# Optimization experiments

Hardware: AMD Instinct MI355X
Metric: run time of the kernel (lower is better)

## Reference

```python
import jax, jax.numpy as jnp
import numpy as np

B, S, E = 32, 577, 1024
H = 16
D = E // H  # head_size = 64


def setup_inputs() -> dict:
    key = jax.random.key(0)
    ks = jax.random.split(key, 5)
    scale_init = E ** -0.5
    x = jax.random.normal(ks[0], (B, S, E), dtype=jnp.float32)
    # Per-head projection weights. torch Linear weight is [out,in]; we store
    # [H, E, D] so that x @ Wq[h] == torch_linear(x) with weight Wq[h].T.
    Wq = jax.random.normal(ks[1], (H, E, D), dtype=jnp.float32) * scale_init
    Wk = jax.random.normal(ks[2], (H, E, D), dtype=jnp.float32) * scale_init
    Wv = jax.random.normal(ks[3], (H, E, D), dtype=jnp.float32) * scale_init
    # Output projection (with bias, as in nn.Linear default)
    Wo = jax.random.normal(ks[4], (E, E), dtype=jnp.float32) * scale_init
    bo = jnp.zeros((E,), dtype=jnp.float32)
    return {"x": x, "Wq": Wq, "Wk": Wk, "Wv": Wv, "Wo": Wo, "bo": bo}


def reference(x, Wq, Wk, Wv, Wo, bo):
    scale = D ** -0.5
    # Per-head QKV projections, vectorized over heads: [B,H,S,D]
    q = jnp.einsum('bse,hed->bhsd', x, Wq)
    k = jnp.einsum('bse,hed->bhsd', x, Wk)
    v = jnp.einsum('bse,hed->bhsd', x, Wv)
    scores = jnp.einsum('bhsd,bhtd->bhst', q, k) * scale  # [B,H,S,S]
    attn = jax.nn.softmax(scores, axis=-1)
    out = jnp.einsum('bhst,bhtd->bhsd', attn, v)  # [B,H,S,D]
    # Concat heads: head h occupies slice [h*D:(h+1)*D], matching torch.cat order
    out = out.transpose(0, 2, 1, 3).reshape(B, S, E)
    return out @ Wo.T + bo  # torch Linear: x @ W.T + b
```

## Files before the change

### kernel.cpp

```cpp
#include <hip/hip_runtime.h>
#include <hip/hip_bf16.h>
#include <stdint.h>

using sh8    = __attribute__((ext_vector_type(8))) short;
using f32x4  = __attribute__((ext_vector_type(4))) float;
using f32x16 = __attribute__((ext_vector_type(16))) float;

#define MFMA16(a, b, c) __builtin_amdgcn_mfma_f32_16x16x32_bf16(a, b, c, 0, 0, 0)
#define EXP2F(x) __builtin_amdgcn_exp2f(x)
#define PRIO1() __builtin_amdgcn_s_setprio(1)
#define PRIO0() __builtin_amdgcn_s_setprio(0)

static constexpr int BB = 32, SS = 577, HH = 16;
static constexpr int MM = BB * SS;
static constexpr int SPAD = 640;
static constexpr float QSCALE = 0.18033688011112042f;

__device__ __forceinline__ ushort f2b(float f) {
  union { float f; uint32_t u; } v{f};
  uint32_t r = v.u + 0x7FFFu + ((v.u >> 16) & 1u);
  return (ushort)(r >> 16);
}

__device__ __forceinline__ float bf2f(ushort u) {
  union { uint32_t u; float f; } v{(uint32_t)u << 16};
  return v.f;
}

#if __has_builtin(__builtin_amdgcn_cvt_pk_bf16_f32)
typedef __attribute__((ext_vector_type(2))) __bf16 bf16x2_t;
__device__ __forceinline__ uint32_t pk_bf16(float a, float b) {
  union { bf16x2_t v; uint32_t u; } c;
  c.v = __builtin_amdgcn_cvt_pk_bf16_f32(a, b);
  return c.u;
}
#else
__device__ __forceinline__ uint32_t pk_bf16(float a, float b) {
  return (uint32_t)f2b(a) | ((uint32_t)f2b(b) << 16);
}
#endif

__device__ __forceinline__ void gld16(const ushort* g, ushort* l) {
  __builtin_amdgcn_global_load_lds(
      (const __attribute__((address_space(1))) uint32_t*)g,
      (__attribute__((address_space(3))) uint32_t*)l, 16, 0, 0);
}

__global__ __launch_bounds__(256)
void convert2_f32_bf16(const float* __restrict__ a, ushort* __restrict__ oa, int na4,
                       const float* __restrict__ b, ushort* __restrict__ ob, int nb4) {
  const int total = na4 + nb4;
  const int stride = gridDim.x * 256;
  for (int i = blockIdx.x * 256 + threadIdx.x; i < total; i += stride) {
    const float4 f = (i < na4) ? ((const float4*)a)[i] : ((const float4*)b)[i - na4];
    ushort4 u;
    u.x = f2b(f.x); u.y = f2b(f.y); u.z = f2b(f.z); u.w = f2b(f.w);
    if (i < na4) ((ushort4*)oa)[i] = u;
    else         ((ushort4*)ob)[i - na4] = u;
  }
}

__global__ __launch_bounds__(256)
void convert_wqkv(const float* __restrict__ Wq, const float* __restrict__ Wk,
                  const float* __restrict__ Wv, ushort* __restrict__ Wt) {
  __shared__ ushort T[64 * 72];
  const int tid = threadIdx.x;
  const int kt = blockIdx.x, sh = blockIdx.y;
  const int sel = sh >> 4, h = sh & 15;
  const float* W = (sel == 0) ? Wq : ((sel == 1) ? Wk : Wv);
  const float qs = (sel == 0) ? QSCALE : 1.0f;
  const int rr = tid >> 4;
  const int rc = (tid & 15) * 4;
#pragma unroll
  for (int p = 0; p < 64; p += 16) {
    const float4 f = *(const float4*)(W + (size_t)h * 65536 + (size_t)(kt * 64 + p + rr) * 64 + rc);
    ushort4 u;
    u.x = f2b(f.x * qs); u.y = f2b(f.y * qs); u.z = f2b(f.z * qs); u.w = f2b(f.w * qs);
    *(ushort4*)&T[(p + rr) * 72 + rc] = u;
  }
  __syncthreads();
  const int dd = tid >> 2;
  const int c16 = (tid & 3) * 16;
  sh8 v0, v1;
#pragma unroll
  for (int j = 0; j < 8; j++) v0[j] = (short)T[(c16 + j) * 72 + dd];
#pragma unroll
  for (int j = 0; j < 8; j++) v1[j] = (short)T[(c16 + 8 + j) * 72 + dd];
  ushort* op = Wt + ((size_t)sel * 1024 + h * 64 + dd) * 1024 + kt * 64 + c16;
  *(sh8*)op = v0;
  *(sh8*)(op + 8) = v1;
}

template <int MODE>
__global__ __launch_bounds__(256)
void gemm_bt(const ushort* __restrict__ A, const ushort* __restrict__ Bt,
             ushort* __restrict__ Cb, float* __restrict__ Cf,
             const float* __restrict__ bias, int M, int N, int K) {
  __shared__ ushort Al[128 * 64];
  __shared__ ushort Bl[128 * 64];
  const int tid = threadIdx.x;
  const int lane = tid & 63, w = tid >> 6;
  const int l15 = lane & 15, quad = lane >> 4;
  const int wm = (w >> 1) * 64, wn = (w & 1) * 64;
  const int m0 = blockIdx.y * 128, n0 = blockIdx.x * 128;

  f32x4 acc[4][4];
#pragma unroll
  for (int i = 0; i < 4; i++)
#pragma unroll
    for (int j = 0; j < 4; j++) acc[i][j] = f32x4{0.f, 0.f, 0.f, 0.f};

  const int rbase = tid >> 3;
  const int swzc = ((tid & 7) ^ (rbase & 7)) * 8;
  const ushort* Ag[4]; const ushort* Bg[4];
  ushort* lA[4]; ushort* lB[4];
#pragma unroll
  for (int i = 0; i < 4; i++) {
    Ag[i] = A + (size_t)min(m0 + i * 32 + rbase, M - 1) * K + swzc;
    Bg[i] = Bt + (size_t)(n0 + i * 32 + rbase) * K + swzc;
    lA[i] = &Al[(i * 256 + tid) * 8];
    lB[i] = &Bl[(i * 256 + tid) * 8];
  }
  const int swz = l15 & 7;
  const int c0 = (quad ^ swz) * 8;
  const int c1 = ((quad + 4) ^ swz) * 8;
  const int arow = (wm + l15) * 64;
  const int brow = (wn + l15) * 64;

  for (int k0 = 0; k0 < K; k0 += 64) {
    __syncthreads();
#pragma unroll
    for (int i = 0; i < 4; i++) {
      gld16(Ag[i] + k0, lA[i]);
      gld16(Bg[i] + k0, lB[i]);
    }
    __syncthreads();
#pragma unroll
    for (int kc = 0; kc < 2; kc++) {
      const int ck = (kc == 0) ? c0 : c1;
      sh8 af[4], bfr[4];
#pragma unroll
      for (int i = 0; i < 4; i++) af[i] = *(const sh8*)&Al[arow + i * 1024 + ck];
#pragma unroll
      for (int j = 0; j < 4; j++) bfr[j] = *(const sh8*)&Bl[brow + j * 1024 + ck];
#pragma unroll
      for (int i = 0; i < 4; i++)
#pragma unroll
        for (int j = 0; j < 4; j++) acc[i][j] = MFMA16(bfr[j], af[i], acc[i][j]);
    }
  }

#pragma unroll
  for (int i = 0; i < 4; i++) {
    const int row = m0 + wm + i * 16 + l15;
    const bool ok = row < M;
#pragma unroll
    for (int j = 0; j < 4; j++) {
      const int col0 = n0 + wn + j * 16 + quad * 4;
      if (MODE == 0) {
        uint2 pk;
        pk.x = pk_bf16(acc[i][j][0], acc[i][j][1]);
        pk.y = pk_bf16(acc[i][j][2], acc[i][j][3]);
        if (ok) *(uint2*)&Cb[(size_t)row * N + col0] = pk;
      } else {
        const float4 b4 = *(const float4*)&bias[col0];
        float4 v;
        v.x = acc[i][j][0] + b4.x; v.y = acc[i][j][1] + b4.y;
        v.z = acc[i][j][2] + b4.z; v.w = acc[i][j][3] + b4.w;
        if (ok) *(float4*)&Cf[(size_t)row * N + col0] = v;
      }
    }
  }
}

__global__ __launch_bounds__(256)
void transpose_v(const ushort* __restrict__ QKV, ushort* __restrict__ Vtg) {
  __shared__ ushort T[64 * 72];
  const int tid = threadIdx.x;
  const int st = blockIdx.x, bh = blockIdx.y;
  const int b = bh >> 4, h = bh & 15;
  const int sr = tid >> 3;
  const int sc = (tid & 7) * 8;
#pragma unroll
  for (int p = 0; p < 64; p += 32) {
    const int s = st * 64 + p + sr;
    uint4 d = uint4{0u, 0u, 0u, 0u};
    if (s < SS) d = *(const uint4*)(QKV + ((size_t)b * SS + s) * 3072 + 2048 + h * 64 + sc);
    *(uint4*)&T[(p + sr) * 72 + sc] = d;
  }
  __syncthreads();
  const int dd = tid >> 2;
  const int s16 = (tid & 3) * 16;
  sh8 v0, v1;
#pragma unroll
  for (int j = 0; j < 8; j++) v0[j] = (short)T[(s16 + j) * 72 + dd];
#pragma unroll
  for (int j = 0; j < 8; j++) v1[j] = (short)T[(s16 + 8 + j) * 72 + dd];
  ushort* outp = Vtg + ((size_t)bh * 64 + dd) * SPAD + st * 64 + s16;
  *(sh8*)outp = v0;
  *(sh8*)(outp + 8) = v1;
}

__global__ __launch_bounds__(256)
void flash_attn(const ushort* __restrict__ QKV, const ushort* __restrict__ Vtg,
                ushort* __restrict__ Ob) {
  __shared__ ushort Kl[2][64 * 64];
  __shared__ ushort Vl[2][64 * 64];
  __shared__ ushort Pl[128 * 72];
  __shared__ ushort vt576[64];
  const int tid = threadIdx.x;
  const int lane = tid & 63, w = tid >> 6;
  const int l15 = lane & 15, quad = lane >> 4;
  const int qb = blockIdx.x, bh = blockIdx.y;
  const int b = bh >> 4, h = bh & 15;

  sh8 qf[2][2];
#pragma unroll
  for (int g = 0; g < 2; g++) {
    const int qr = qb * 128 + w * 32 + g * 16 + l15;
    const ushort* qrow = QKV + ((size_t)b * SS + min(qr, SS - 1)) * 3072 + h * 64;
    qf[g][0] = *(const sh8*)(qrow + quad * 8);
    qf[g][1] = *(const sh8*)(qrow + 32 + quad * 8);
  }

  sh8 ones;
#pragma unroll
  for (int j = 0; j < 8; j++) ones[j] = (short)0x3F80;

  f32x4 o[2][4];
  f32x4 acc_l[2];
#pragma unroll
  for (int g = 0; g < 2; g++) {
    acc_l[g] = f32x4{0.f, 0.f, 0.f, 0.f};
#pragma unroll
    for (int t = 0; t < 4; t++) o[g][t] = f32x4{0.f, 0.f, 0.f, 0.f};
  }

  const int r0 = tid >> 3;
  const int swzs = ((tid & 7) ^ (r0 & 7)) * 8;
  const ushort* Kg = QKV + (size_t)b * SS * 3072 + 1024 + h * 64 + swzs;
  const ushort* Vg0 = Vtg + ((size_t)bh * 64 + r0) * SPAD + swzs;
  const ushort* Vg1 = Vtg + ((size_t)bh * 64 + 32 + r0) * SPAD + swzs;
  ushort* lK0[2] = { &Kl[0][tid * 8],         &Kl[1][tid * 8] };
  ushort* lK1[2] = { &Kl[0][(256 + tid) * 8], &Kl[1][(256 + tid) * 8] };
  ushort* lV0[2] = { &Vl[0][tid * 8],         &Vl[1][tid * 8] };
  ushort* lV1[2] = { &Vl[0][(256 + tid) * 8], &Vl[1][(256 + tid) * 8] };

  const int swz = l15 & 7;
  const int ca0 = (quad ^ swz) * 8;
  const int ca1 = ((quad + 4) ^ swz) * 8;
  ushort* plw[2] = { &Pl[(w * 32 + l15) * 72], &Pl[(w * 32 + 16 + l15) * 72] };

  gld16(Kg + (size_t)r0 * 3072, lK0[0]);
  gld16(Kg + (size_t)(32 + r0) * 3072, lK1[0]);
  gld16(Vg0, lV0[0]);
  gld16(Vg1, lV1[0]);
  if (tid < 64) vt576[tid] = QKV[((size_t)b * SS + 576) * 3072 + 2048 + h * 64 + tid];
  __syncthreads();

  for (int kt = 0; kt < 9; kt++) {
    const int cur = kt & 1;
    if (kt < 8) {
      const int kb1 = (kt + 1) * 64;
      gld16(Kg + (size_t)(kb1 + r0) * 3072, lK0[cur ^ 1]);
      gld16(Kg + (size_t)(kb1 + 32 + r0) * 3072, lK1[cur ^ 1]);
      gld16(Vg0 + kb1, lV0[cur ^ 1]);
      gld16(Vg1 + kb1, lV1[cur ^ 1]);
    }
    const ushort* Kc = &Kl[cur][0];
    const ushort* Vc = &Vl[cur][0];

#pragma unroll
    for (int tn = 0; tn < 4; tn++) {
      const int kr = tn * 16 + l15;
      const sh8 k0 = *(const sh8*)&Kc[kr * 64 + ca0];
      const sh8 k1 = *(const sh8*)&Kc[kr * 64 + ca1];
      f32x4 sv[2];
      PRIO1();
#pragma unroll
      for (int g = 0; g < 2; g++) {
        sv[g] = f32x4{0.f, 0.f, 0.f, 0.f};
        sv[g] = MFMA16(k0, qf[g][0], sv[g]);
        sv[g] = MFMA16(k1, qf[g][1], sv[g]);
      }
      PRIO0();
#pragma unroll
      for (int g = 0; g < 2; g++) {
        uint2 pp;
        pp.x = pk_bf16(EXP2F(sv[g][0]), EXP2F(sv[g][1]));
        pp.y = pk_bf16(EXP2F(sv[g][2]), EXP2F(sv[g][3]));
        *(uint2*)(plw[g] + tn * 16 + quad * 4) = pp;
      }
    }
    sh8 pa[2][2];
#pragma unroll
    for (int g = 0; g < 2; g++) {
      pa[g][0] = *(const sh8*)(plw[g] + quad * 8);
      pa[g][1] = *(const sh8*)(plw[g] + 32 + quad * 8);
    }
    PRIO1();
#pragma unroll
    for (int g = 0; g < 2; g++) {
      acc_l[g] = MFMA16(ones, pa[g][0], acc_l[g]);
      acc_l[g] = MFMA16(ones, pa[g][1], acc_l[g]);
    }
#pragma unroll
    for (int t = 0; t < 4; t++) {
      const int vr = t * 16 + l15;
      const sh8 v0 = *(const sh8*)&Vc[vr * 64 + ca0];
      const sh8 v1 = *(const sh8*)&Vc[vr * 64 + ca1];
#pragma unroll
      for (int g = 0; g < 2; g++) {
        o[g][t] = MFMA16(v0, pa[g][0], o[g][t]);
        o[g][t] = MFMA16(v1, pa[g][1], o[g][t]);
      }
    }
    PRIO0();

    if (kt < 8) __syncthreads();
  }

  const ushort* k576p = QKV + ((size_t)b * SS + 576) * 3072 + 1024 + h * 64;
  const sh8 kta = *(const sh8*)(k576p + quad * 8);
  const sh8 ktb = *(const sh8*)(k576p + 32 + quad * 8);
  float p5[2];
#pragma unroll
  for (int g = 0; g < 2; g++) {
    float s = 0.f;
#pragma unroll
    for (int j = 0; j < 8; j++) {
      s += bf2f((ushort)qf[g][0][j]) * bf2f((ushort)kta[j]);
      s += bf2f((ushort)qf[g][1][j]) * bf2f((ushort)ktb[j]);
    }
    s += __shfl_xor(s, 16);
    s += __shfl_xor(s, 32);
    p5[g] = EXP2F(s);
  }
#pragma unroll
  for (int g = 0; g < 2; g++)
#pragma unroll
    for (int t = 0; t < 4; t++)
#pragma unroll
      for (int r = 0; r < 4; r++)
        o[g][t][r] += p5[g] * bf2f(vt576[t * 16 + quad * 4 + r]);

#pragma unroll
  for (int g = 0; g < 2; g++) {
    const float inv = 1.0f / (acc_l[g][0] + p5[g]);
    const int s = qb * 128 + w * 32 + g * 16 + l15;
    if (s < SS) {
      ushort* op = Ob + ((size_t)b * SS + s) * 1024 + h * 64 + quad * 4;
#pragma unroll
      for (int t = 0; t < 4; t++) {
        uint2 ov;
        ov.x = pk_bf16(o[g][t][0] * inv, o[g][t][1] * inv);
        ov.y = pk_bf16(o[g][t][2] * inv, o[g][t][3] * inv);
        *(uint2*)(op + t * 16) = ov;
      }
    }
  }
}

extern "C" void kernel_launch(void* const* d_in, const int* in_sizes, int n_in,
                              void* d_out, int out_size, void* d_ws, size_t ws_size,
                              hipStream_t stream) {
  const float* x  = (const float*)d_in[0];
  const float* Wq = (const float*)d_in[1];
  const float* Wk = (const float*)d_in[2];
  const float* Wv = (const float*)d_in[3];
  const float* Wo = (const float*)d_in[4];
  const float* bo = (const float*)d_in[5];
  float* out = (float*)d_out;

  ushort* Xb  = (ushort*)d_ws;
  ushort* Wt  = Xb  + (size_t)MM * 1024;
  ushort* Wob = Wt  + (size_t)3072 * 1024;
  ushort* QKV = Wob + (size_t)1024 * 1024;
  ushort* Vtg = QKV + (size_t)MM * 3072;
  ushort* Ob  = Xb;

  convert2_f32_bf16<<<4096, 256, 0, stream>>>(x, Xb, MM * 1024 / 4, Wo, Wob, 1024 * 1024 / 4);
  convert_wqkv<<<dim3(16, 48), 256, 0, stream>>>(Wq, Wk, Wv, Wt);
  gemm_bt<0><<<dim3(24, 145), 256, 0, stream>>>(Xb, Wt, QKV, nullptr, nullptr, MM, 3072, 1024);
  transpose_v<<<dim3(10, 512), 256, 0, stream>>>(QKV, Vtg);
  flash_attn<<<dim3(5, 512), 256, 0, stream>>>(QKV, Vtg, Ob);
  gemm_bt<1><<<dim3(8, 145), 256, 0, stream>>>(Ob, Wob, nullptr, out, bo, MM, 1024, 1024);
}
```

Baseline: 426.1 us.

## Fuse V transpose into QKV GEMM epilogue and merge conversion kernels

The QKV projection GEMM now writes the V columns directly in transposed [bh][d][s] layout by staging the tile through shared memory, which removes the separate transpose_v kernel and its read/write of V. The two f32->bf16 conversion kernels are merged into one launch, with the block index choosing weight transpose or elementwise conversion. The costs are an extra LDS round trip and barriers in the V-tile epilogue, plus scalar fallback writes at sequence boundaries. Padding columns of Vtg beyond 577 are no longer zero-filled, and flash_attn now reads the last V row from Vtg.

```diff
diff --git a/kernel.cpp b/kernel.cpp
--- a/kernel.cpp
+++ b/kernel.cpp
@@ -47,57 +47,61 @@
 }
 
 __global__ __launch_bounds__(256)
-void convert2_f32_bf16(const float* __restrict__ a, ushort* __restrict__ oa, int na4,
-                       const float* __restrict__ b, ushort* __restrict__ ob, int nb4) {
-  const int total = na4 + nb4;
-  const int stride = gridDim.x * 256;
-  for (int i = blockIdx.x * 256 + threadIdx.x; i < total; i += stride) {
-    const float4 f = (i < na4) ? ((const float4*)a)[i] : ((const float4*)b)[i - na4];
-    ushort4 u;
-    u.x = f2b(f.x); u.y = f2b(f.y); u.z = f2b(f.z); u.w = f2b(f.w);
-    if (i < na4) ((ushort4*)oa)[i] = u;
-    else         ((ushort4*)ob)[i - na4] = u;
-  }
-}
-
-__global__ __launch_bounds__(256)
-void convert_wqkv(const float* __restrict__ Wq, const float* __restrict__ Wk,
-                  const float* __restrict__ Wv, ushort* __restrict__ Wt) {
+void convert_all(const float* __restrict__ x, ushort* __restrict__ Xb,
+                 const float* __restrict__ Wo, ushort* __restrict__ Wob,
+                 const float* __restrict__ Wq, const float* __restrict__ Wk,
+                 const float* __restrict__ Wv, ushort* __restrict__ Wt) {
   __shared__ ushort T[64 * 72];
   const int tid = threadIdx.x;
-  const int kt = blockIdx.x, sh = blockIdx.y;
-  const int sel = sh >> 4, h = sh & 15;
-  const float* W = (sel == 0) ? Wq : ((sel == 1) ? Wk : Wv);
-  const float qs = (sel == 0) ? QSCALE : 1.0f;
-  const int rr = tid >> 4;
-  const int rc = (tid & 15) * 4;
-#pragma unroll
-  for (int p = 0; p < 64; p += 16) {
-    const float4 f = *(const float4*)(W + (size_t)h * 65536 + (size_t)(kt * 64 + p + rr) * 64 + rc);
-    ushort4 u;
-    u.x = f2b(f.x * qs); u.y = f2b(f.y * qs); u.z = f2b(f.z * qs); u.w = f2b(f.w * qs);
-    *(ushort4*)&T[(p + rr) * 72 + rc] = u;
-  }
-  __syncthreads();
-  const int dd = tid >> 2;
-  const int c16 = (tid & 3) * 16;
-  sh8 v0, v1;
-#pragma unroll
-  for (int j = 0; j < 8; j++) v0[j] = (short)T[(c16 + j) * 72 + dd];
-#pragma unroll
-  for (int j = 0; j < 8; j++) v1[j] = (short)T[(c16 + 8 + j) * 72 + dd];
-  ushort* op = Wt + ((size_t)sel * 1024 + h * 64 + dd) * 1024 + kt * 64 + c16;
-  *(sh8*)op = v0;
-  *(sh8*)(op + 8) = v1;
+  const int blk = blockIdx.x;
+  if (blk < 768) {
+    const int kt = blk & 15, sh = blk >> 4;
+    const int sel = sh >> 4, h = sh & 15;
+    const float* W = (sel == 0) ? Wq : ((sel == 1) ? Wk : Wv);
+    const float qs = (sel == 0) ? QSCALE : 1.0f;
+    const int rr = tid >> 4;
+    const int rc = (tid & 15) * 4;
+#pragma unroll
+    for (int p = 0; p < 64; p += 16) {
+      const float4 f = *(const float4*)(W + (size_t)h * 65536 + (size_t)(kt * 64 + p + rr) * 64 + rc);
+      ushort4 u;
+      u.x = f2b(f.x * qs); u.y = f2b(f.y * qs); u.z = f2b(f.z * qs); u.w = f2b(f.w * qs);
+      *(ushort4*)&T[(p + rr) * 72 + rc] = u;
+    }
+    __syncthreads();
+    const int dd = tid >> 2;
+    const int c16 = (tid & 3) * 16;
+    sh8 v0, v1;
+#pragma unroll
+    for (int j = 0; j < 8; j++) v0[j] = (short)T[(c16 + j) * 72 + dd];
+#pragma unroll
+    for (int j = 0; j < 8; j++) v1[j] = (short)T[(c16 + 8 + j) * 72 + dd];
+    ushort* op = Wt + ((size_t)sel * 1024 + h * 64 + dd) * 1024 + kt * 64 + c16;
+    *(sh8*)op = v0;
+    *(sh8*)(op + 8) = v1;
+  } else {
+    const int na4 = MM * 1024 / 4, nb4 = 1024 * 1024 / 4;
+    const int total = na4 + nb4;
+    const int stride = (gridDim.x - 768) * 256;
+    for (int i = (blk - 768) * 256 + tid; i < total; i += stride) {
+      const float4 f = (i < na4) ? ((const float4*)x)[i] : ((const float4*)Wo)[i - na4];
+      ushort4 u;
+      u.x = f2b(f.x); u.y = f2b(f.y); u.z = f2b(f.z); u.w = f2b(f.w);
+      if (i < na4) ((ushort4*)Xb)[i] = u;
+      else         ((ushort4*)Wob)[i - na4] = u;
+    }
+  }
 }
 
 template <int MODE>
 __global__ __launch_bounds__(256)
 void gemm_bt(const ushort* __restrict__ A, const ushort* __restrict__ Bt,
              ushort* __restrict__ Cb, float* __restrict__ Cf,
-             const float* __restrict__ bias, int M, int N, int K) {
-  __shared__ ushort Al[128 * 64];
-  __shared__ ushort Bl[128 * 64];
+             const float* __restrict__ bias, ushort* __restrict__ Vout,
+             int M, int N, int K) {
+  __shared__ ushort SH[128 * 128];
+  ushort* Al = SH;
+  ushort* Bl = SH + 128 * 64;
   const int tid = threadIdx.x;
   const int lane = tid & 63, w = tid >> 6;
   const int l15 = lane & 15, quad = lane >> 4;
@@ -150,55 +154,70 @@
     }
   }
 
-#pragma unroll
-  for (int i = 0; i < 4; i++) {
-    const int row = m0 + wm + i * 16 + l15;
-    const bool ok = row < M;
-#pragma unroll
-    for (int j = 0; j < 4; j++) {
-      const int col0 = n0 + wn + j * 16 + quad * 4;
-      if (MODE == 0) {
-        uint2 pk;
-        pk.x = pk_bf16(acc[i][j][0], acc[i][j][1]);
-        pk.y = pk_bf16(acc[i][j][2], acc[i][j][3]);
-        if (ok) *(uint2*)&Cb[(size_t)row * N + col0] = pk;
+  if (MODE == 0 && n0 >= 2048) {
+    __syncthreads();
+#pragma unroll
+    for (int i = 0; i < 4; i++) {
+      const int ml = wm + i * 16 + l15;
+#pragma unroll
+      for (int j = 0; j < 4; j++) {
+#pragma unroll
+        for (int r = 0; r < 4; r++) {
+          const int nl = wn + j * 16 + quad * 4 + r;
+          SH[nl * 128 + (ml ^ (((nl >> 2) & 7) << 1))] = f2b(acc[i][j][r]);
+        }
+      }
+    }
+    __syncthreads();
+    const int nl = tid >> 1;
+    const int half = tid & 1;
+    const int cg = n0 - 2048 + nl;
+    const int h = cg >> 6, d = cg & 63;
+    const int xs = ((nl >> 2) & 7) << 1;
+    const ushort* Trow = SH + nl * 128;
+    int m = m0 + half * 64;
+    const int mhi = min(m + 64, MM);
+    int b = m / 577;
+    int s = m - b * 577;
+    ushort* vrow = Vout + ((size_t)((b << 4) + h) * 64 + d) * SPAD;
+    while (m < mhi) {
+      int take = 8 - (s & 7);
+      take = min(take, 577 - s);
+      take = min(take, mhi - m);
+      if (take == 8) {
+        ushort tmp[8];
+#pragma unroll
+        for (int e = 0; e < 8; e++) tmp[e] = Trow[(m - m0 + e) ^ xs];
+        *(sh8*)(vrow + s) = *(const sh8*)tmp;
       } else {
-        const float4 b4 = *(const float4*)&bias[col0];
-        float4 v;
-        v.x = acc[i][j][0] + b4.x; v.y = acc[i][j][1] + b4.y;
-        v.z = acc[i][j][2] + b4.z; v.w = acc[i][j][3] + b4.w;
-        if (ok) *(float4*)&Cf[(size_t)row * N + col0] = v;
-      }
-    }
-  }
-}
-
-__global__ __launch_bounds__(256)
-void transpose_v(const ushort* __restrict__ QKV, ushort* __restrict__ Vtg) {
-  __shared__ ushort T[64 * 72];
-  const int tid = threadIdx.x;
-  const int st = blockIdx.x, bh = blockIdx.y;
-  const int b = bh >> 4, h = bh & 15;
-  const int sr = tid >> 3;
-  const int sc = (tid & 7) * 8;
-#pragma unroll
-  for (int p = 0; p < 64; p += 32) {
-    const int s = st * 64 + p + sr;
-    uint4 d = uint4{0u, 0u, 0u, 0u};
-    if (s < SS) d = *(const uint4*)(QKV + ((size_t)b * SS + s) * 3072 + 2048 + h * 64 + sc);
-    *(uint4*)&T[(p + sr) * 72 + sc] = d;
-  }
-  __syncthreads();
-  const int dd = tid >> 2;
-  const int s16 = (tid & 3) * 16;
-  sh8 v0, v1;
-#pragma unroll
-  for (int j = 0; j < 8; j++) v0[j] = (short)T[(s16 + j) * 72 + dd];
-#pragma unroll
-  for (int j = 0; j < 8; j++) v1[j] = (short)T[(s16 + 8 + j) * 72 + dd];
-  ushort* outp = Vtg + ((size_t)bh * 64 + dd) * SPAD + st * 64 + s16;
-  *(sh8*)outp = v0;
-  *(sh8*)(outp + 8) = v1;
+        for (int e = 0; e < take; e++) vrow[s + e] = Trow[(m - m0 + e) ^ xs];
+      }
+      m += take; s += take;
+      if (s == 577) { s = 0; b++; vrow = Vout + ((size_t)((b << 4) + h) * 64 + d) * SPAD; }
+    }
+  } else {
+#pragma unroll
+    for (int i = 0; i < 4; i++) {
+      const int row = m0 + wm + i * 16 + l15;
+      const bool ok = row < M;
+#pragma unroll
+      for (int j = 0; j < 4; j++) {
+        const int col0 = n0 + wn + j * 16 + quad * 4;
+        if (MODE == 0) {
+          uint2 pk;
+          pk.x = pk_bf16(acc[i][j][0], acc[i][j][1]);
+          pk.y = pk_bf16(acc[i][j][2], acc[i][j][3]);
+          if (ok) *(uint2*)&Cb[(size_t)row * N + col0] = pk;
+        } else {
+          const float4 b4 = *(const float4*)&bias[col0];
+          float4 v;
+          v.x = acc[i][j][0] + b4.x; v.y = acc[i][j][1] + b4.y;
+          v.z = acc[i][j][2] + b4.z; v.w = acc[i][j][3] + b4.w;
+          if (ok) *(float4*)&Cf[(size_t)row * N + col0] = v;
+        }
+      }
+    }
+  }
 }
 
 __global__ __launch_bounds__(256)
@@ -255,7 +274,7 @@
   gld16(Kg + (size_t)(32 + r0) * 3072, lK1[0]);
   gld16(Vg0, lV0[0]);
   gld16(Vg1, lV1[0]);
-  if (tid < 64) vt576[tid] = QKV[((size_t)b * SS + 576) * 3072 + 2048 + h * 64 + tid];
+  if (tid < 64) vt576[tid] = Vtg[((size_t)bh * 64 + tid) * SPAD + 576];
   __syncthreads();
 
   for (int kt = 0; kt < 9; kt++) {
@@ -379,10 +398,8 @@
   ushort* Vtg = QKV + (size_t)MM * 3072;
   ushort* Ob  = Xb;
 
-  convert2_f32_bf16<<<4096, 256, 0, stream>>>(x, Xb, MM * 1024 / 4, Wo, Wob, 1024 * 1024 / 4);
-  convert_wqkv<<<dim3(16, 48), 256, 0, stream>>>(Wq, Wk, Wv, Wt);
-  gemm_bt<0><<<dim3(24, 145), 256, 0, stream>>>(Xb, Wt, QKV, nullptr, nullptr, MM, 3072, 1024);
-  transpose_v<<<dim3(10, 512), 256, 0, stream>>>(QKV, Vtg);
+  convert_all<<<4096, 256, 0, stream>>>(x, Xb, Wo, Wob, Wq, Wk, Wv, Wt);
+  gemm_bt<0><<<dim3(24, 145), 256, 0, stream>>>(Xb, Wt, QKV, nullptr, nullptr, Vtg, MM, 3072, 1024);
   flash_attn<<<dim3(5, 512), 256, 0, stream>>>(QKV, Vtg, Ob);
-  gemm_bt<1><<<dim3(8, 145), 256, 0, stream>>>(Ob, Wob, nullptr, out, bo, MM, 1024, 1024);
-}
+  gemm_bt<1><<<dim3(8, 145), 256, 0, stream>>>(Ob, Wob, nullptr, out, bo, nullptr, MM, 1024, 1024);
+}
```

Result: slower. 439.1 us (+3.1%).
